# Kernel tuning notes

Measured on AMD Instinct MI355X. Metric: run time of the kernel, lower is better.

## Reference

```python
import jax, jax.numpy as jnp
import numpy as np

B, F, HID, NH, KS, BS = 64, 1024, 2048, 4, 4, 4
HD = HID // NH          # 512 head dim in mLSTMCell
NB = HID // BS          # 512 block-diagonal blocks for q/k/v proj
EPS = 1e-6


def setup_inputs() -> dict:
    key = jax.random.key(0)
    ks = jax.random.split(key, 10)
    r = lambda i, shape, s=0.02: jax.random.normal(ks[i], shape, jnp.float32) * s
    return {
        "inputs": jax.random.normal(ks[0], (B, F), jnp.float32),
        # recurrent carry (zeros_init per _initialize_carry)
        "C": jnp.zeros((B, NH, HD, HD), jnp.float32),
        "n": jnp.zeros((B, NH, HD, 1), jnp.float32),
        "m": jnp.zeros((B, NH, 1, 1), jnp.float32),
        "conv_state": jnp.zeros((B, KS, HID), jnp.float32),
        # parameters
        "W_up": r(1, (F, 2 * HID)),            # up_proj, no bias
        "conv_w": r(2, (KS, HID)),             # depthwise causal conv
        "conv_b": jnp.zeros((HID,), jnp.float32),
        "Wq": r(3, (NB, BS, BS)),              # block-diagonal projections
        "Wk": r(4, (NB, BS, BS)),
        "Wv": r(5, (NB, BS, BS)),
        "Wi": jnp.zeros((3 * HID, NH), jnp.float32),   # gate kernels init to zero
        "bi": jax.random.normal(ks[6], (NH,), jnp.float32) * 0.1,
        "Wf": jnp.zeros((3 * HID, NH), jnp.float32),
        "bf": jnp.linspace(3.0, 6.0, NH, dtype=jnp.float32),  # linspace_init(3,6)
        "norm_scale": jnp.ones((NH, HD), jnp.float32),  # MultiHeadLayerNorm scale
        "skip": jnp.ones((HID,), jnp.float32),          # learnable_skip
        "W_down": r(7, (HID, F)),
    }


def reference(inputs, C, n, m, conv_state, W_up, conv_w, conv_b,
              Wq, Wk, Wv, Wi, bi, Wf, bf, norm_scale, skip, W_down):
    x = inputs[:, None, :]                               # (B,1,F)  add_time_axis
    up = x @ W_up                                        # (B,1,2*HID)
    x, z = jnp.split(up, 2, axis=-1)                     # each (B,1,HID)

    # causal depthwise conv1d, single step: shift state, append x
    conv_state_new = jnp.concatenate([conv_state[:, 1:], x], axis=1)   # (B,KS,HID)
    conv_x = jnp.einsum('bkh,kh->bh', conv_state_new, conv_w)[:, None, :] + conv_b
    conv_x_act = jax.nn.silu(conv_x)                     # (B,1,HID)

    def blockdiag(t, W):  # block-diagonal dense: NB blocks of BSxBS
        tb = t.reshape(B, 1, NB, BS)
        return jnp.einsum('bsnd,nde->bsne', tb, W).reshape(B, 1, HID)

    q = blockdiag(conv_x_act, Wq)
    k = blockdiag(conv_x_act, Wk)
    v = blockdiag(x, Wv)

    # ---- mLSTMCell ----
    qkv = jnp.concatenate([q, k, v], axis=-1)            # (B,1,3*HID)
    qh = q.reshape(B, NH, HD, 1)
    kh = k.reshape(B, NH, HD, 1) / jnp.sqrt(jnp.float32(HD))
    vh = v.reshape(B, NH, HD, 1)

    i_tilde = (qkv @ Wi + bi).swapaxes(-1, -2)[..., None]   # (B,NH,1,1)
    f_tilde = (qkv @ Wf + bf).swapaxes(-1, -2)[..., None]   # (B,NH,1,1)
    log_f = -jax.nn.softplus(-f_tilde)
    m_new = jnp.maximum(log_f + m, i_tilde)
    i_p = jnp.exp(i_tilde - m_new)
    f_p = jnp.exp(log_f + m - m_new)

    C_new = f_p * C + i_p * (kh @ vh.swapaxes(-1, -2))   # rank-1 update (B,NH,HD,HD)
    n_new = f_p * n + i_p * kh                           # (B,NH,HD,1)

    nom = qh.swapaxes(-1, -2) @ C_new                    # (B,NH,1,HD)
    den = jnp.maximum(jnp.abs(qh.swapaxes(-1, -2) @ n_new), jnp.exp(-m_new))
    h_tilde = nom / (den + EPS)                          # (B,NH,1,HD)

    # MultiHeadLayerNorm over head_dim, scale only
    mu = h_tilde.mean(-1, keepdims=True)
    var = h_tilde.var(-1, keepdims=True)
    h_norm = (h_tilde - mu) * jax.lax.rsqrt(var + EPS) * norm_scale[None, :, None, :]
    h_norm = h_norm.swapaxes(1, 2).reshape(B, 1, HID)    # (B,1,HID)
    # ---- end cell ----

    h = h_norm + skip * conv_x_act
    h = h * jax.nn.silu(z)
    y = (h @ W_down)[:, 0]                               # remove_time_axis -> (B,F)
    return (y, C_new, n_new, m_new, conv_state_new)
```

## Files before the change

### kernel.cpp

```cpp
#include <hip/hip_runtime.h>
#include <math.h>

#define BB   64
#define FF   1024
#define HIDD 2048
#define NHH  4
#define KSS  4
#define HDD  512
#define EPSV 1e-6f
#define INV_SQRT_HD 0.04419417382415922f

__global__ __launch_bounds__(256) void k_up_part(const float* __restrict__ A,
                                                 const float* __restrict__ W,
                                                 float* __restrict__ part) {
    const int tid = threadIdx.x;
    const int c  = blockIdx.x * 256 + tid;
    const int b0 = blockIdx.y * 16;
    const int k0 = blockIdx.z * 256;
    __shared__ float As[16 * 256];
#pragma unroll
    for (int j = 0; j < 16; ++j)
        As[j * 256 + tid] = A[(size_t)(b0 + j) * FF + k0 + tid];
    __syncthreads();
    float acc[16];
#pragma unroll
    for (int i = 0; i < 16; ++i) acc[i] = 0.f;
    const float* __restrict__ wp = W + (size_t)k0 * (2 * HIDD) + c;
#pragma unroll 4
    for (int f = 0; f < 256; ++f) {
        const float w = wp[(size_t)f * (2 * HIDD)];
#pragma unroll
        for (int i = 0; i < 16; ++i) acc[i] += As[i * 256 + f] * w;
    }
    float* __restrict__ pp = part + ((size_t)blockIdx.z * BB + b0) * (2 * HIDD) + c;
#pragma unroll
    for (int i = 0; i < 16; ++i) pp[(size_t)i * (2 * HIDD)] = acc[i];
}

__global__ __launch_bounds__(256) void k_up_red(const float* __restrict__ part,
                                                float* __restrict__ up) {
    const int i = (blockIdx.x * 256 + threadIdx.x) * 4;
    float4 s = *(const float4*)(part + i);
#pragma unroll
    for (int kc = 1; kc < 4; ++kc) {
        const float4 p = *(const float4*)(part + (size_t)kc * BB * 2 * HIDD + i);
        s.x += p.x; s.y += p.y; s.z += p.z; s.w += p.w;
    }
    *(float4*)(up + i) = s;
}

__global__ __launch_bounds__(512) void k_conv_qkv(
    const float* __restrict__ up, const float* __restrict__ conv_state,
    const float* __restrict__ conv_w, const float* __restrict__ conv_b,
    const float* __restrict__ Wq, const float* __restrict__ Wk, const float* __restrict__ Wv,
    float* __restrict__ out_cs, float* __restrict__ act,
    float* __restrict__ qb, float* __restrict__ kb, float* __restrict__ vb) {
    const int b  = blockIdx.x;
    const int n  = threadIdx.x;
    const int h0 = n * 4;
    const float4 x4  = *(const float4*)(up + (size_t)b*(2*HIDD) + h0);
    const float4 cs1 = *(const float4*)(conv_state + (size_t)b*KSS*HIDD + 1*HIDD + h0);
    const float4 cs2 = *(const float4*)(conv_state + (size_t)b*KSS*HIDD + 2*HIDD + h0);
    const float4 cs3 = *(const float4*)(conv_state + (size_t)b*KSS*HIDD + 3*HIDD + h0);
    *(float4*)(out_cs + (size_t)b*KSS*HIDD + 0*HIDD + h0) = cs1;
    *(float4*)(out_cs + (size_t)b*KSS*HIDD + 1*HIDD + h0) = cs2;
    *(float4*)(out_cs + (size_t)b*KSS*HIDD + 2*HIDD + h0) = cs3;
    *(float4*)(out_cs + (size_t)b*KSS*HIDD + 3*HIDD + h0) = x4;
    const float4 w0 = *(const float4*)(conv_w + 0*HIDD + h0);
    const float4 w1 = *(const float4*)(conv_w + 1*HIDD + h0);
    const float4 w2 = *(const float4*)(conv_w + 2*HIDD + h0);
    const float4 w3 = *(const float4*)(conv_w + 3*HIDD + h0);
    const float4 cb = *(const float4*)(conv_b + h0);
    float4 cx;
    cx.x = cs1.x*w0.x + cs2.x*w1.x + cs3.x*w2.x + x4.x*w3.x + cb.x;
    cx.y = cs1.y*w0.y + cs2.y*w1.y + cs3.y*w2.y + x4.y*w3.y + cb.y;
    cx.z = cs1.z*w0.z + cs2.z*w1.z + cs3.z*w2.z + x4.z*w3.z + cb.z;
    cx.w = cs1.w*w0.w + cs2.w*w1.w + cs3.w*w2.w + x4.w*w3.w + cb.w;
    float4 a4;
    a4.x = cx.x / (1.f + expf(-cx.x));
    a4.y = cx.y / (1.f + expf(-cx.y));
    a4.z = cx.z / (1.f + expf(-cx.z));
    a4.w = cx.w / (1.f + expf(-cx.w));
    *(float4*)(act + (size_t)b*HIDD + h0) = a4;

    const float4 q0 = *(const float4*)(Wq + (size_t)n*16 + 0);
    const float4 q1 = *(const float4*)(Wq + (size_t)n*16 + 4);
    const float4 q2 = *(const float4*)(Wq + (size_t)n*16 + 8);
    const float4 q3 = *(const float4*)(Wq + (size_t)n*16 + 12);
    float4 q4;
    q4.x = a4.x*q0.x + a4.y*q1.x + a4.z*q2.x + a4.w*q3.x;
    q4.y = a4.x*q0.y + a4.y*q1.y + a4.z*q2.y + a4.w*q3.y;
    q4.z = a4.x*q0.z + a4.y*q1.z + a4.z*q2.z + a4.w*q3.z;
    q4.w = a4.x*q0.w + a4.y*q1.w + a4.z*q2.w + a4.w*q3.w;
    *(float4*)(qb + (size_t)b*HIDD + h0) = q4;
    const float4 k0 = *(const float4*)(Wk + (size_t)n*16 + 0);
    const float4 k1 = *(const float4*)(Wk + (size_t)n*16 + 4);
    const float4 k2 = *(const float4*)(Wk + (size_t)n*16 + 8);
    const float4 k3 = *(const float4*)(Wk + (size_t)n*16 + 12);
    float4 k4;
    k4.x = a4.x*k0.x + a4.y*k1.x + a4.z*k2.x + a4.w*k3.x;
    k4.y = a4.x*k0.y + a4.y*k1.y + a4.z*k2.y + a4.w*k3.y;
    k4.z = a4.x*k0.z + a4.y*k1.z + a4.z*k2.z + a4.w*k3.z;
    k4.w = a4.x*k0.w + a4.y*k1.w + a4.z*k2.w + a4.w*k3.w;
    *(float4*)(kb + (size_t)b*HIDD + h0) = k4;
    const float4 v0 = *(const float4*)(Wv + (size_t)n*16 + 0);
    const float4 v1 = *(const float4*)(Wv + (size_t)n*16 + 4);
    const float4 v2 = *(const float4*)(Wv + (size_t)n*16 + 8);
    const float4 v3 = *(const float4*)(Wv + (size_t)n*16 + 12);
    float4 v4;
    v4.x = x4.x*v0.x + x4.y*v1.x + x4.z*v2.x + x4.w*v3.x;
    v4.y = x4.x*v0.y + x4.y*v1.y + x4.z*v2.y + x4.w*v3.y;
    v4.z = x4.x*v0.z + x4.y*v1.z + x4.z*v2.z + x4.w*v3.z;
    v4.w = x4.x*v0.w + x4.y*v1.w + x4.z*v2.w + x4.w*v3.w;
    *(float4*)(vb + (size_t)b*HIDD + h0) = v4;
}

__global__ __launch_bounds__(256) void k_gates(
    const float* __restrict__ qb, const float* __restrict__ kb, const float* __restrict__ vb,
    const float* __restrict__ Wi, const float* __restrict__ bi,
    const float* __restrict__ Wf, const float* __restrict__ bf,
    const float* __restrict__ mstate_in, const float* __restrict__ nstate_in,
    float* __restrict__ out_m, float* __restrict__ out_n, float* __restrict__ scal) {
    const int bh = blockIdx.x, b = bh >> 2, h = bh & 3;
    const int tid = threadIdx.x;
    __shared__ float r1[256], r2[256];
    __shared__ float bc[3];
    float si = 0.f, sf = 0.f;
    for (int j = tid; j < 3*HIDD; j += 256) {
        const float val = (j < HIDD) ? qb[(size_t)b*HIDD + j]
                        : (j < 2*HIDD) ? kb[(size_t)b*HIDD + j - HIDD]
                                       : vb[(size_t)b*HIDD + j - 2*HIDD];
        si += val * Wi[(size_t)j*NHH + h];
        sf += val * Wf[(size_t)j*NHH + h];
    }
    r1[tid] = si; r2[tid] = sf; __syncthreads();
    for (int s = 128; s > 0; s >>= 1) {
        if (tid < s) { r1[tid] += r1[tid+s]; r2[tid] += r2[tid+s]; }
        __syncthreads();
    }
    if (tid == 0) {
        const float i_t = r1[0] + bi[h];
        const float f_t = r2[0] + bf[h];
        const float log_f = fminf(f_t, 0.f) - log1pf(expf(-fabsf(f_t)));
        const float m_old = mstate_in[bh];
        const float m_new = fmaxf(log_f + m_old, i_t);
        out_m[bh] = m_new;
        bc[0] = expf(log_f + m_old - m_new);
        bc[1] = expf(i_t - m_new) * INV_SQRT_HD;
        bc[2] = expf(-m_new);
    }
    __syncthreads();
    const float f_p = bc[0], ik = bc[1];
    float qn = 0.f;
#pragma unroll
    for (int t = 0; t < 2; ++t) {
        const int d = tid + t*256;
        const float nn = f_p * nstate_in[(size_t)bh*HDD + d] + ik * kb[(size_t)b*HIDD + h*HDD + d];
        out_n[(size_t)bh*HDD + d] = nn;
        qn += qb[(size_t)b*HIDD + h*HDD + d] * nn;
    }
    __syncthreads();
    r1[tid] = qn; __syncthreads();
    for (int s = 128; s > 0; s >>= 1) {
        if (tid < s) r1[tid] += r1[tid+s];
        __syncthreads();
    }
    if (tid == 0) {
        const float den = fmaxf(fabsf(r1[0]), bc[2]);
        scal[bh*4 + 0] = f_p;
        scal[bh*4 + 1] = ik;
        scal[bh*4 + 2] = 1.f / (den + EPSV);
    }
}

__global__ __launch_bounds__(256) void k_cupd(
    const float* __restrict__ C_in, const float* __restrict__ qb,
    const float* __restrict__ kb, const float* __restrict__ vb,
    const float* __restrict__ scal, float* __restrict__ C_out,
    float* __restrict__ nom_part) {
    const int bh = blockIdx.x, rc = blockIdx.y;
    const int b = bh >> 2, h = bh & 3;
    const int tid = threadIdx.x;
    const int c4 = tid & 127, rh = tid >> 7;
    __shared__ float qs[128], ks[128];
    if (tid < 128) qs[tid]      = qb[(size_t)b*HIDD + h*HDD + rc*128 + tid];
    else           ks[tid-128]  = kb[(size_t)b*HIDD + h*HDD + rc*128 + (tid-128)];
    __syncthreads();
    const float f_p = scal[bh*4 + 0], ik = scal[bh*4 + 1];
    const float4 v4 = *(const float4*)(vb + (size_t)b*HIDD + h*HDD + c4*4);
    float4 nom = {0.f,0.f,0.f,0.f};
    const size_t base = ((size_t)bh*HDD + rc*128 + rh*64) * HDD + c4*4;
    const float* __restrict__ cin = C_in + base;
    float* __restrict__ cout = C_out + base;
#pragma unroll 4
    for (int i = 0; i < 64; ++i) {
        const int l = rh*64 + i;
        const float4 c = *(const float4*)(cin + (size_t)i*HDD);
        const float ikk = ik * ks[l];
        float4 cn;
        cn.x = f_p*c.x + ikk*v4.x;
        cn.y = f_p*c.y + ikk*v4.y;
        cn.z = f_p*c.z + ikk*v4.z;
        cn.w = f_p*c.w + ikk*v4.w;
        *(float4*)(cout + (size_t)i*HDD) = cn;
        const float qd = qs[l];
        nom.x += qd*cn.x; nom.y += qd*cn.y; nom.z += qd*cn.z; nom.w += qd*cn.w;
    }
    __shared__ float4 rn[256];
    rn[tid] = nom;
    __syncthreads();
    if (rh == 0) {
        float4 o = rn[tid + 128];
        o.x += nom.x; o.y += nom.y; o.z += nom.z; o.w += nom.w;
        *(float4*)(nom_part + ((size_t)bh*4 + rc)*HDD + c4*4) = o;
    }
}

__global__ __launch_bounds__(256) void k_norm(
    const float* __restrict__ nom_part, const float* __restrict__ scal,
    const float* __restrict__ norm_scale, const float* __restrict__ skip,
    const float* __restrict__ act, const float* __restrict__ up,
    float* __restrict__ hbuf) {
    const int bh = blockIdx.x, b = bh >> 2, h = bh & 3;
    const int tid = threadIdx.x;
    const float invden = scal[bh*4 + 2];
    float ht[2];
    float s = 0.f, sq = 0.f;
#pragma unroll
    for (int t = 0; t < 2; ++t) {
        const int j = tid + t*256;
        float nm = 0.f;
#pragma unroll
        for (int rc = 0; rc < 4; ++rc) nm += nom_part[((size_t)bh*4 + rc)*HDD + j];
        const float v = nm * invden;
        ht[t] = v; s += v; sq += v*v;
    }
    __shared__ float r1[256], r2[256];
    r1[tid] = s; r2[tid] = sq; __syncthreads();
    for (int st = 128; st > 0; st >>= 1) {
        if (tid < st) { r1[tid] += r1[tid+st]; r2[tid] += r2[tid+st]; }
        __syncthreads();
    }
    const float mu = r1[0] * (1.f/HDD);
    const float var = r2[0] * (1.f/HDD) - mu*mu;
    const float rs = rsqrtf(var + EPSV);
#pragma unroll
    for (int t = 0; t < 2; ++t) {
        const int j = tid + t*256;
        const int hid = h*HDD + j;
        const float hn = (ht[t] - mu) * rs * norm_scale[(size_t)h*HDD + j];
        float val = hn + skip[hid] * act[(size_t)b*HIDD + hid];
        const float z = up[(size_t)b*(2*HIDD) + HIDD + hid];
        val *= z / (1.f + expf(-z));
        hbuf[(size_t)b*HIDD + hid] = val;
    }
}

__global__ __launch_bounds__(256) void k_down_part(const float* __restrict__ A,
                                                   const float* __restrict__ W,
                                                   float* __restrict__ part) {
    const int tid = threadIdx.x;
    const int c  = blockIdx.x * 256 + tid;
    const int b0 = blockIdx.y * 16;
    const int k0 = blockIdx.z * 128;
    __shared__ float As[16 * 128];
#pragma unroll
    for (int j = 0; j < 8; ++j) {
        const int e = j * 256 + tid;
        const int i = e >> 7, f = e & 127;
        As[e] = A[(size_t)(b0 + i) * HIDD + k0 + f];
    }
    __syncthreads();
    float acc[16];
#pragma unroll
    for (int i = 0; i < 16; ++i) acc[i] = 0.f;
    const float* __restrict__ wp = W + (size_t)k0 * FF + c;
#pragma unroll 4
    for (int f = 0; f < 128; ++f) {
        const float w = wp[(size_t)f * FF];
#pragma unroll
        for (int i = 0; i < 16; ++i) acc[i] += As[i * 128 + f] * w;
    }
    float* __restrict__ pp = part + ((size_t)blockIdx.z * BB + b0) * FF + c;
#pragma unroll
    for (int i = 0; i < 16; ++i) pp[(size_t)i * FF] = acc[i];
}

__global__ __launch_bounds__(256) void k_down_red(const float* __restrict__ part,
                                                  float* __restrict__ y) {
    const int i = (blockIdx.x * 256 + threadIdx.x) * 4;
    float4 s = *(const float4*)(part + i);
#pragma unroll
    for (int kc = 1; kc < 16; ++kc) {
        const float4 p = *(const float4*)(part + (size_t)kc * BB * FF + i);
        s.x += p.x; s.y += p.y; s.z += p.z; s.w += p.w;
    }
    *(float4*)(y + i) = s;
}

extern "C" void kernel_launch(void* const* d_in, const int* in_sizes, int n_in,
                              void* d_out, int out_size, void* d_ws, size_t ws_size,
                              hipStream_t stream) {
    const float* inputs     = (const float*)d_in[0];
    const float* C_in       = (const float*)d_in[1];
    const float* nstate_in  = (const float*)d_in[2];
    const float* mstate_in  = (const float*)d_in[3];
    const float* conv_state = (const float*)d_in[4];
    const float* W_up       = (const float*)d_in[5];
    const float* conv_w     = (const float*)d_in[6];
    const float* conv_b     = (const float*)d_in[7];
    const float* Wq         = (const float*)d_in[8];
    const float* Wk         = (const float*)d_in[9];
    const float* Wv         = (const float*)d_in[10];
    const float* Wi         = (const float*)d_in[11];
    const float* bi         = (const float*)d_in[12];
    const float* Wf         = (const float*)d_in[13];
    const float* bf         = (const float*)d_in[14];
    const float* norm_scale = (const float*)d_in[15];
    const float* skip       = (const float*)d_in[16];
    const float* W_down     = (const float*)d_in[17];

    float* ws = (float*)d_ws;
    float* up       = ws;
    float* act      = ws + 262144;
    float* qb       = ws + 393216;
    float* kb       = ws + 524288;
    float* vb       = ws + 655360;
    float* scal     = ws + 786432;
    float* nom_part = ws + 787456;
    float* hbuf     = ws + 1311744;
    float* part_up  = ws + 1442816;
    float* part_y   = ws + 2491392;

    float* out_y  = (float*)d_out;
    float* out_C  = out_y + 65536;
    float* out_n  = out_C + 67108864;
    float* out_m  = out_n + 131072;
    float* out_cs = out_m + 256;

    k_up_part <<<dim3(16, 4, 4), 256, 0, stream>>>(inputs, W_up, part_up);
    k_up_red  <<<256,            256, 0, stream>>>(part_up, up);
    k_conv_qkv<<<BB,             512, 0, stream>>>(up, conv_state, conv_w, conv_b,
                                                   Wq, Wk, Wv, out_cs, act, qb, kb, vb);
    k_gates   <<<BB*NHH,         256, 0, stream>>>(qb, kb, vb, Wi, bi, Wf, bf,
                                                   mstate_in, nstate_in, out_m, out_n, scal);
    k_cupd    <<<dim3(BB*NHH, 4), 256, 0, stream>>>(C_in, qb, kb, vb, scal, out_C, nom_part);
    k_norm    <<<BB*NHH,         256, 0, stream>>>(nom_part, scal, norm_scale, skip, act, up, hbuf);
    k_down_part<<<dim3(4, 4, 16), 256, 0, stream>>>(hbuf, W_down, part_y);
    k_down_red <<<64,            256, 0, stream>>>(part_y, out_y);
}
```

Before: 576.1 us.

## Fuse mid-pipeline kernels: up-reduce into conv/qkv/gates, C-update into norm

Folds the up-projection split-K reduction, conv, q/k/v projection, gate computation and n-state update into one per-batch kernel that uses wave shuffles for its reductions. The C rank-1 update is merged with the layer norm and output gating in a 512-thread block per (batch, head), which removes the nom_part round trip. The two GEMM inner loops are also vectorised to read float4 from shared memory. Going from eight launches to five cuts launch overhead and intermediate traffic, but the C update now runs on 256 blocks instead of 1024, which may reduce memory-level parallelism on the dominant 256MB stream.

```diff
diff --git a/kernel.cpp b/kernel.cpp
--- a/kernel.cpp
+++ b/kernel.cpp
@@ -26,233 +26,262 @@
 #pragma unroll
     for (int i = 0; i < 16; ++i) acc[i] = 0.f;
     const float* __restrict__ wp = W + (size_t)k0 * (2 * HIDD) + c;
-#pragma unroll 4
-    for (int f = 0; f < 256; ++f) {
-        const float w = wp[(size_t)f * (2 * HIDD)];
-#pragma unroll
-        for (int i = 0; i < 16; ++i) acc[i] += As[i * 256 + f] * w;
+#pragma unroll 2
+    for (int f4 = 0; f4 < 64; ++f4) {
+        const float w0 = wp[(size_t)(4*f4 + 0) * (2 * HIDD)];
+        const float w1 = wp[(size_t)(4*f4 + 1) * (2 * HIDD)];
+        const float w2 = wp[(size_t)(4*f4 + 2) * (2 * HIDD)];
+        const float w3 = wp[(size_t)(4*f4 + 3) * (2 * HIDD)];
+#pragma unroll
+        for (int i = 0; i < 16; ++i) {
+            const float4 a = *(const float4*)(As + i * 256 + f4 * 4);
+            acc[i] += a.x * w0 + a.y * w1 + a.z * w2 + a.w * w3;
+        }
     }
     float* __restrict__ pp = part + ((size_t)blockIdx.z * BB + b0) * (2 * HIDD) + c;
 #pragma unroll
     for (int i = 0; i < 16; ++i) pp[(size_t)i * (2 * HIDD)] = acc[i];
 }
 
-__global__ __launch_bounds__(256) void k_up_red(const float* __restrict__ part,
-                                                float* __restrict__ up) {
-    const int i = (blockIdx.x * 256 + threadIdx.x) * 4;
-    float4 s = *(const float4*)(part + i);
-#pragma unroll
-    for (int kc = 1; kc < 4; ++kc) {
-        const float4 p = *(const float4*)(part + (size_t)kc * BB * 2 * HIDD + i);
-        s.x += p.x; s.y += p.y; s.z += p.z; s.w += p.w;
-    }
-    *(float4*)(up + i) = s;
-}
-
-__global__ __launch_bounds__(512) void k_conv_qkv(
-    const float* __restrict__ up, const float* __restrict__ conv_state,
+__global__ __launch_bounds__(512) void k_mid(
+    const float* __restrict__ part_up, const float* __restrict__ conv_state,
     const float* __restrict__ conv_w, const float* __restrict__ conv_b,
     const float* __restrict__ Wq, const float* __restrict__ Wk, const float* __restrict__ Wv,
-    float* __restrict__ out_cs, float* __restrict__ act,
-    float* __restrict__ qb, float* __restrict__ kb, float* __restrict__ vb) {
+    const float* __restrict__ Wi, const float* __restrict__ bi,
+    const float* __restrict__ Wf, const float* __restrict__ bf,
+    const float* __restrict__ mstate_in, const float* __restrict__ nstate_in,
+    const float* __restrict__ skip,
+    float* __restrict__ out_cs, float* __restrict__ out_m, float* __restrict__ out_n,
+    float* __restrict__ sact, float* __restrict__ zsil,
+    float* __restrict__ qb, float* __restrict__ kb, float* __restrict__ vb,
+    float* __restrict__ scal) {
     const int b  = blockIdx.x;
     const int n  = threadIdx.x;
     const int h0 = n * 4;
-    const float4 x4  = *(const float4*)(up + (size_t)b*(2*HIDD) + h0);
-    const float4 cs1 = *(const float4*)(conv_state + (size_t)b*KSS*HIDD + 1*HIDD + h0);
-    const float4 cs2 = *(const float4*)(conv_state + (size_t)b*KSS*HIDD + 2*HIDD + h0);
-    const float4 cs3 = *(const float4*)(conv_state + (size_t)b*KSS*HIDD + 3*HIDD + h0);
-    *(float4*)(out_cs + (size_t)b*KSS*HIDD + 0*HIDD + h0) = cs1;
-    *(float4*)(out_cs + (size_t)b*KSS*HIDD + 1*HIDD + h0) = cs2;
-    *(float4*)(out_cs + (size_t)b*KSS*HIDD + 2*HIDD + h0) = cs3;
-    *(float4*)(out_cs + (size_t)b*KSS*HIDD + 3*HIDD + h0) = x4;
-    const float4 w0 = *(const float4*)(conv_w + 0*HIDD + h0);
-    const float4 w1 = *(const float4*)(conv_w + 1*HIDD + h0);
-    const float4 w2 = *(const float4*)(conv_w + 2*HIDD + h0);
-    const float4 w3 = *(const float4*)(conv_w + 3*HIDD + h0);
-    const float4 cb = *(const float4*)(conv_b + h0);
+
+    float4 x4 = *(const float4*)(part_up + (size_t)b * (2 * HIDD) + h0);
+#pragma unroll
+    for (int kc = 1; kc < 4; ++kc) {
+        const float4 p = *(const float4*)(part_up + ((size_t)kc * BB + b) * (2 * HIDD) + h0);
+        x4.x += p.x; x4.y += p.y; x4.z += p.z; x4.w += p.w;
+    }
+    float4 z4 = *(const float4*)(part_up + (size_t)b * (2 * HIDD) + HIDD + h0);
+#pragma unroll
+    for (int kc = 1; kc < 4; ++kc) {
+        const float4 p = *(const float4*)(part_up + ((size_t)kc * BB + b) * (2 * HIDD) + HIDD + h0);
+        z4.x += p.x; z4.y += p.y; z4.z += p.z; z4.w += p.w;
+    }
+    float4 zs;
+    zs.x = z4.x / (1.f + expf(-z4.x));
+    zs.y = z4.y / (1.f + expf(-z4.y));
+    zs.z = z4.z / (1.f + expf(-z4.z));
+    zs.w = z4.w / (1.f + expf(-z4.w));
+    *(float4*)(zsil + (size_t)b * HIDD + h0) = zs;
+
+    const float4 cs1 = *(const float4*)(conv_state + (size_t)b * KSS * HIDD + 1 * HIDD + h0);
+    const float4 cs2 = *(const float4*)(conv_state + (size_t)b * KSS * HIDD + 2 * HIDD + h0);
+    const float4 cs3 = *(const float4*)(conv_state + (size_t)b * KSS * HIDD + 3 * HIDD + h0);
+    *(float4*)(out_cs + (size_t)b * KSS * HIDD + 0 * HIDD + h0) = cs1;
+    *(float4*)(out_cs + (size_t)b * KSS * HIDD + 1 * HIDD + h0) = cs2;
+    *(float4*)(out_cs + (size_t)b * KSS * HIDD + 2 * HIDD + h0) = cs3;
+    *(float4*)(out_cs + (size_t)b * KSS * HIDD + 3 * HIDD + h0) = x4;
+    const float4 cw0 = *(const float4*)(conv_w + 0 * HIDD + h0);
+    const float4 cw1 = *(const float4*)(conv_w + 1 * HIDD + h0);
+    const float4 cw2 = *(const float4*)(conv_w + 2 * HIDD + h0);
+    const float4 cw3 = *(const float4*)(conv_w + 3 * HIDD + h0);
+    const float4 cb  = *(const float4*)(conv_b + h0);
     float4 cx;
-    cx.x = cs1.x*w0.x + cs2.x*w1.x + cs3.x*w2.x + x4.x*w3.x + cb.x;
-    cx.y = cs1.y*w0.y + cs2.y*w1.y + cs3.y*w2.y + x4.y*w3.y + cb.y;
-    cx.z = cs1.z*w0.z + cs2.z*w1.z + cs3.z*w2.z + x4.z*w3.z + cb.z;
-    cx.w = cs1.w*w0.w + cs2.w*w1.w + cs3.w*w2.w + x4.w*w3.w + cb.w;
+    cx.x = cs1.x*cw0.x + cs2.x*cw1.x + cs3.x*cw2.x + x4.x*cw3.x + cb.x;
+    cx.y = cs1.y*cw0.y + cs2.y*cw1.y + cs3.y*cw2.y + x4.y*cw3.y + cb.y;
+    cx.z = cs1.z*cw0.z + cs2.z*cw1.z + cs3.z*cw2.z + x4.z*cw3.z + cb.z;
+    cx.w = cs1.w*cw0.w + cs2.w*cw1.w + cs3.w*cw2.w + x4.w*cw3.w + cb.w;
     float4 a4;
     a4.x = cx.x / (1.f + expf(-cx.x));
     a4.y = cx.y / (1.f + expf(-cx.y));
     a4.z = cx.z / (1.f + expf(-cx.z));
     a4.w = cx.w / (1.f + expf(-cx.w));
-    *(float4*)(act + (size_t)b*HIDD + h0) = a4;
-
-    const float4 q0 = *(const float4*)(Wq + (size_t)n*16 + 0);
-    const float4 q1 = *(const float4*)(Wq + (size_t)n*16 + 4);
-    const float4 q2 = *(const float4*)(Wq + (size_t)n*16 + 8);
-    const float4 q3 = *(const float4*)(Wq + (size_t)n*16 + 12);
-    float4 q4;
-    q4.x = a4.x*q0.x + a4.y*q1.x + a4.z*q2.x + a4.w*q3.x;
-    q4.y = a4.x*q0.y + a4.y*q1.y + a4.z*q2.y + a4.w*q3.y;
-    q4.z = a4.x*q0.z + a4.y*q1.z + a4.z*q2.z + a4.w*q3.z;
-    q4.w = a4.x*q0.w + a4.y*q1.w + a4.z*q2.w + a4.w*q3.w;
-    *(float4*)(qb + (size_t)b*HIDD + h0) = q4;
-    const float4 k0 = *(const float4*)(Wk + (size_t)n*16 + 0);
-    const float4 k1 = *(const float4*)(Wk + (size_t)n*16 + 4);
-    const float4 k2 = *(const float4*)(Wk + (size_t)n*16 + 8);
-    const float4 k3 = *(const float4*)(Wk + (size_t)n*16 + 12);
-    float4 k4;
-    k4.x = a4.x*k0.x + a4.y*k1.x + a4.z*k2.x + a4.w*k3.x;
-    k4.y = a4.x*k0.y + a4.y*k1.y + a4.z*k2.y + a4.w*k3.y;
-    k4.z = a4.x*k0.z + a4.y*k1.z + a4.z*k2.z + a4.w*k3.z;
-    k4.w = a4.x*k0.w + a4.y*k1.w + a4.z*k2.w + a4.w*k3.w;
-    *(float4*)(kb + (size_t)b*HIDD + h0) = k4;
-    const float4 v0 = *(const float4*)(Wv + (size_t)n*16 + 0);
-    const float4 v1 = *(const float4*)(Wv + (size_t)n*16 + 4);
-    const float4 v2 = *(const float4*)(Wv + (size_t)n*16 + 8);
-    const float4 v3 = *(const float4*)(Wv + (size_t)n*16 + 12);
-    float4 v4;
-    v4.x = x4.x*v0.x + x4.y*v1.x + x4.z*v2.x + x4.w*v3.x;
-    v4.y = x4.x*v0.y + x4.y*v1.y + x4.z*v2.y + x4.w*v3.y;
-    v4.z = x4.x*v0.z + x4.y*v1.z + x4.z*v2.z + x4.w*v3.z;
-    v4.w = x4.x*v0.w + x4.y*v1.w + x4.z*v2.w + x4.w*v3.w;
-    *(float4*)(vb + (size_t)b*HIDD + h0) = v4;
-}
-
-__global__ __launch_bounds__(256) void k_gates(
-    const float* __restrict__ qb, const float* __restrict__ kb, const float* __restrict__ vb,
-    const float* __restrict__ Wi, const float* __restrict__ bi,
-    const float* __restrict__ Wf, const float* __restrict__ bf,
-    const float* __restrict__ mstate_in, const float* __restrict__ nstate_in,
-    float* __restrict__ out_m, float* __restrict__ out_n, float* __restrict__ scal) {
+    const float4 sk = *(const float4*)(skip + h0);
+    float4 sa;
+    sa.x = sk.x * a4.x; sa.y = sk.y * a4.y; sa.z = sk.z * a4.z; sa.w = sk.w * a4.w;
+    *(float4*)(sact + (size_t)b * HIDD + h0) = sa;
+
+    const float4 q0 = *(const float4*)(Wq + (size_t)n * 16 + 0);
+    const float4 q1 = *(const float4*)(Wq + (size_t)n * 16 + 4);
+    const float4 q2 = *(const float4*)(Wq + (size_t)n * 16 + 8);
+    const float4 q3 = *(const float4*)(Wq + (size_t)n * 16 + 12);
+    float4 qv4;
+    qv4.x = a4.x*q0.x + a4.y*q1.x + a4.z*q2.x + a4.w*q3.x;
+    qv4.y = a4.x*q0.y + a4.y*q1.y + a4.z*q2.y + a4.w*q3.y;
+    qv4.z = a4.x*q0.z + a4.y*q1.z + a4.z*q2.z + a4.w*q3.z;
+    qv4.w = a4.x*q0.w + a4.y*q1.w + a4.z*q2.w + a4.w*q3.w;
+    *(float4*)(qb + (size_t)b * HIDD + h0) = qv4;
+    const float4 k0v = *(const float4*)(Wk + (size_t)n * 16 + 0);
+    const float4 k1v = *(const float4*)(Wk + (size_t)n * 16 + 4);
+    const float4 k2v = *(const float4*)(Wk + (size_t)n * 16 + 8);
+    const float4 k3v = *(const float4*)(Wk + (size_t)n * 16 + 12);
+    float4 kv4;
+    kv4.x = a4.x*k0v.x + a4.y*k1v.x + a4.z*k2v.x + a4.w*k3v.x;
+    kv4.y = a4.x*k0v.y + a4.y*k1v.y + a4.z*k2v.y + a4.w*k3v.y;
+    kv4.z = a4.x*k0v.z + a4.y*k1v.z + a4.z*k2v.z + a4.w*k3v.z;
+    kv4.w = a4.x*k0v.w + a4.y*k1v.w + a4.z*k2v.w + a4.w*k3v.w;
+    *(float4*)(kb + (size_t)b * HIDD + h0) = kv4;
+    const float4 v0 = *(const float4*)(Wv + (size_t)n * 16 + 0);
+    const float4 v1 = *(const float4*)(Wv + (size_t)n * 16 + 4);
+    const float4 v2 = *(const float4*)(Wv + (size_t)n * 16 + 8);
+    const float4 v3 = *(const float4*)(Wv + (size_t)n * 16 + 12);
+    float4 vv4;
+    vv4.x = x4.x*v0.x + x4.y*v1.x + x4.z*v2.x + x4.w*v3.x;
+    vv4.y = x4.x*v0.y + x4.y*v1.y + x4.z*v2.y + x4.w*v3.y;
+    vv4.z = x4.x*v0.z + x4.y*v1.z + x4.z*v2.z + x4.w*v3.z;
+    vv4.w = x4.x*v0.w + x4.y*v1.w + x4.z*v2.w + x4.w*v3.w;
+    *(float4*)(vb + (size_t)b * HIDD + h0) = vv4;
+
+    float si0 = 0.f, si1 = 0.f, si2 = 0.f, si3 = 0.f;
+    float sf0 = 0.f, sf1 = 0.f, sf2 = 0.f, sf3 = 0.f;
+#define GATE_R(comp, r) { \
+    const float qr = qv4.comp, kr = kv4.comp, vr = vv4.comp; \
+    const float4 wq_ = *(const float4*)(Wi + (size_t)(h0 + (r)) * NHH); \
+    const float4 wk_ = *(const float4*)(Wi + (size_t)(HIDD + h0 + (r)) * NHH); \
+    const float4 wv_ = *(const float4*)(Wi + (size_t)(2*HIDD + h0 + (r)) * NHH); \
+    si0 += qr*wq_.x + kr*wk_.x + vr*wv_.x; \
+    si1 += qr*wq_.y + kr*wk_.y + vr*wv_.y; \
+    si2 += qr*wq_.z + kr*wk_.z + vr*wv_.z; \
+    si3 += qr*wq_.w + kr*wk_.w + vr*wv_.w; \
+    const float4 fq_ = *(const float4*)(Wf + (size_t)(h0 + (r)) * NHH); \
+    const float4 fk_ = *(const float4*)(Wf + (size_t)(HIDD + h0 + (r)) * NHH); \
+    const float4 fv_ = *(const float4*)(Wf + (size_t)(2*HIDD + h0 + (r)) * NHH); \
+    sf0 += qr*fq_.x + kr*fk_.x + vr*fv_.x; \
+    sf1 += qr*fq_.y + kr*fk_.y + vr*fv_.y; \
+    sf2 += qr*fq_.z + kr*fk_.z + vr*fv_.z; \
+    sf3 += qr*fq_.w + kr*fk_.w + vr*fv_.w; \
+}
+    GATE_R(x, 0) GATE_R(y, 1) GATE_R(z, 2) GATE_R(w, 3)
+#undef GATE_R
+#pragma unroll
+    for (int off = 32; off > 0; off >>= 1) {
+        si0 += __shfl_down(si0, off); si1 += __shfl_down(si1, off);
+        si2 += __shfl_down(si2, off); si3 += __shfl_down(si3, off);
+        sf0 += __shfl_down(sf0, off); sf1 += __shfl_down(sf1, off);
+        sf2 += __shfl_down(sf2, off); sf3 += __shfl_down(sf3, off);
+    }
+    const int lane = n & 63, wv = n >> 6;
+    __shared__ float Ls[8][8];
+    if (lane == 0) {
+        Ls[wv][0] = si0; Ls[wv][1] = si1; Ls[wv][2] = si2; Ls[wv][3] = si3;
+        Ls[wv][4] = sf0; Ls[wv][5] = sf1; Ls[wv][6] = sf2; Ls[wv][7] = sf3;
+    }
+    __syncthreads();
+    __shared__ float bcst[4][3];
+    if (n < 4) {
+        float it = bi[n], ft = bf[n];
+#pragma unroll
+        for (int w = 0; w < 8; ++w) { it += Ls[w][n]; ft += Ls[w][4 + n]; }
+        const float log_f = fminf(ft, 0.f) - log1pf(expf(-fabsf(ft)));
+        const float m_old = mstate_in[b * NHH + n];
+        const float m_new = fmaxf(log_f + m_old, it);
+        out_m[b * NHH + n] = m_new;
+        const float f_p = expf(log_f + m_old - m_new);
+        const float ikv = expf(it - m_new) * INV_SQRT_HD;
+        bcst[n][0] = f_p; bcst[n][1] = ikv; bcst[n][2] = expf(-m_new);
+        float* sc = scal + (size_t)(b * NHH + n) * 4;
+        sc[0] = f_p; sc[1] = ikv;
+    }
+    __syncthreads();
+
+    const int h  = n >> 7;
+    const int bh = b * NHH + h;
+    const float f_p = bcst[h][0], ikv = bcst[h][1];
+    const int d0 = (n & 127) * 4;
+    const float4 nin = *(const float4*)(nstate_in + (size_t)bh * HDD + d0);
+    float4 nn;
+    nn.x = f_p * nin.x + ikv * kv4.x;
+    nn.y = f_p * nin.y + ikv * kv4.y;
+    nn.z = f_p * nin.z + ikv * kv4.z;
+    nn.w = f_p * nin.w + ikv * kv4.w;
+    *(float4*)(out_n + (size_t)bh * HDD + d0) = nn;
+    float qn = qv4.x * nn.x + qv4.y * nn.y + qv4.z * nn.z + qv4.w * nn.w;
+#pragma unroll
+    for (int off = 32; off > 0; off >>= 1) qn += __shfl_down(qn, off);
+    __shared__ float qnl[8];
+    if (lane == 0) qnl[wv] = qn;
+    __syncthreads();
+    if (n < 4) {
+        const float den = fmaxf(fabsf(qnl[2 * n] + qnl[2 * n + 1]), bcst[n][2]);
+        scal[(size_t)(b * NHH + n) * 4 + 2] = 1.f / (den + EPSV);
+    }
+}
+
+__global__ __launch_bounds__(512) void k_cupd_norm(
+    const float* __restrict__ C_in, const float* __restrict__ qb,
+    const float* __restrict__ kb, const float* __restrict__ vb,
+    const float* __restrict__ scal, const float* __restrict__ norm_scale,
+    const float* __restrict__ sact, const float* __restrict__ zsil,
+    float* __restrict__ C_out, float* __restrict__ hbuf) {
     const int bh = blockIdx.x, b = bh >> 2, h = bh & 3;
     const int tid = threadIdx.x;
-    __shared__ float r1[256], r2[256];
-    __shared__ float bc[3];
-    float si = 0.f, sf = 0.f;
-    for (int j = tid; j < 3*HIDD; j += 256) {
-        const float val = (j < HIDD) ? qb[(size_t)b*HIDD + j]
-                        : (j < 2*HIDD) ? kb[(size_t)b*HIDD + j - HIDD]
-                                       : vb[(size_t)b*HIDD + j - 2*HIDD];
-        si += val * Wi[(size_t)j*NHH + h];
-        sf += val * Wf[(size_t)j*NHH + h];
-    }
-    r1[tid] = si; r2[tid] = sf; __syncthreads();
-    for (int s = 128; s > 0; s >>= 1) {
-        if (tid < s) { r1[tid] += r1[tid+s]; r2[tid] += r2[tid+s]; }
-        __syncthreads();
-    }
-    if (tid == 0) {
-        const float i_t = r1[0] + bi[h];
-        const float f_t = r2[0] + bf[h];
-        const float log_f = fminf(f_t, 0.f) - log1pf(expf(-fabsf(f_t)));
-        const float m_old = mstate_in[bh];
-        const float m_new = fmaxf(log_f + m_old, i_t);
-        out_m[bh] = m_new;
-        bc[0] = expf(log_f + m_old - m_new);
-        bc[1] = expf(i_t - m_new) * INV_SQRT_HD;
-        bc[2] = expf(-m_new);
-    }
-    __syncthreads();
-    const float f_p = bc[0], ik = bc[1];
-    float qn = 0.f;
-#pragma unroll
-    for (int t = 0; t < 2; ++t) {
-        const int d = tid + t*256;
-        const float nn = f_p * nstate_in[(size_t)bh*HDD + d] + ik * kb[(size_t)b*HIDD + h*HDD + d];
-        out_n[(size_t)bh*HDD + d] = nn;
-        qn += qb[(size_t)b*HIDD + h*HDD + d] * nn;
-    }
-    __syncthreads();
-    r1[tid] = qn; __syncthreads();
-    for (int s = 128; s > 0; s >>= 1) {
-        if (tid < s) r1[tid] += r1[tid+s];
-        __syncthreads();
-    }
-    if (tid == 0) {
-        const float den = fmaxf(fabsf(r1[0]), bc[2]);
-        scal[bh*4 + 0] = f_p;
-        scal[bh*4 + 1] = ik;
-        scal[bh*4 + 2] = 1.f / (den + EPSV);
-    }
-}
-
-__global__ __launch_bounds__(256) void k_cupd(
-    const float* __restrict__ C_in, const float* __restrict__ qb,
-    const float* __restrict__ kb, const float* __restrict__ vb,
-    const float* __restrict__ scal, float* __restrict__ C_out,
-    float* __restrict__ nom_part) {
-    const int bh = blockIdx.x, rc = blockIdx.y;
-    const int b = bh >> 2, h = bh & 3;
-    const int tid = threadIdx.x;
-    const int c4 = tid & 127, rh = tid >> 7;
-    __shared__ float qs[128], ks[128];
-    if (tid < 128) qs[tid]      = qb[(size_t)b*HIDD + h*HDD + rc*128 + tid];
-    else           ks[tid-128]  = kb[(size_t)b*HIDD + h*HDD + rc*128 + (tid-128)];
-    __syncthreads();
-    const float f_p = scal[bh*4 + 0], ik = scal[bh*4 + 1];
-    const float4 v4 = *(const float4*)(vb + (size_t)b*HIDD + h*HDD + c4*4);
-    float4 nom = {0.f,0.f,0.f,0.f};
-    const size_t base = ((size_t)bh*HDD + rc*128 + rh*64) * HDD + c4*4;
-    const float* __restrict__ cin = C_in + base;
+    const int c4 = tid & 127, rg = tid >> 7;
+    __shared__ float qs[HDD], kik[HDD];
+    const float f_p    = scal[bh * 4 + 0];
+    const float ikv    = scal[bh * 4 + 1];
+    const float invden = scal[bh * 4 + 2];
+    qs[tid]  = qb[(size_t)b * HIDD + h * HDD + tid];
+    kik[tid] = ikv * kb[(size_t)b * HIDD + h * HDD + tid];
+    __syncthreads();
+    const float4 v4 = *(const float4*)(vb + (size_t)b * HIDD + h * HDD + c4 * 4);
+    float4 nom = {0.f, 0.f, 0.f, 0.f};
+    const size_t base = ((size_t)bh * HDD + rg * 128) * HDD + c4 * 4;
+    const float* __restrict__ cin  = C_in  + base;
     float* __restrict__ cout = C_out + base;
-#pragma unroll 4
-    for (int i = 0; i < 64; ++i) {
-        const int l = rh*64 + i;
-        const float4 c = *(const float4*)(cin + (size_t)i*HDD);
-        const float ikk = ik * ks[l];
+#pragma unroll 8
+    for (int i = 0; i < 128; ++i) {
+        const float4 c = *(const float4*)(cin + (size_t)i * HDD);
+        const float kk = kik[rg * 128 + i];
         float4 cn;
-        cn.x = f_p*c.x + ikk*v4.x;
-        cn.y = f_p*c.y + ikk*v4.y;
-        cn.z = f_p*c.z + ikk*v4.z;
-        cn.w = f_p*c.w + ikk*v4.w;
-        *(float4*)(cout + (size_t)i*HDD) = cn;
-        const float qd = qs[l];
-        nom.x += qd*cn.x; nom.y += qd*cn.y; nom.z += qd*cn.z; nom.w += qd*cn.w;
-    }
-    __shared__ float4 rn[256];
+        cn.x = f_p * c.x + kk * v4.x;
+        cn.y = f_p * c.y + kk * v4.y;
+        cn.z = f_p * c.z + kk * v4.z;
+        cn.w = f_p * c.w + kk * v4.w;
+        *(float4*)(cout + (size_t)i * HDD) = cn;
+        const float qd = qs[rg * 128 + i];
+        nom.x += qd * cn.x; nom.y += qd * cn.y; nom.z += qd * cn.z; nom.w += qd * cn.w;
+    }
+    __shared__ float4 rn[512];
     rn[tid] = nom;
     __syncthreads();
-    if (rh == 0) {
-        float4 o = rn[tid + 128];
-        o.x += nom.x; o.y += nom.y; o.z += nom.z; o.w += nom.w;
-        *(float4*)(nom_part + ((size_t)bh*4 + rc)*HDD + c4*4) = o;
-    }
-}
-
-__global__ __launch_bounds__(256) void k_norm(
-    const float* __restrict__ nom_part, const float* __restrict__ scal,
-    const float* __restrict__ norm_scale, const float* __restrict__ skip,
-    const float* __restrict__ act, const float* __restrict__ up,
-    float* __restrict__ hbuf) {
-    const int bh = blockIdx.x, b = bh >> 2, h = bh & 3;
-    const int tid = threadIdx.x;
-    const float invden = scal[bh*4 + 2];
-    float ht[2];
-    float s = 0.f, sq = 0.f;
-#pragma unroll
-    for (int t = 0; t < 2; ++t) {
-        const int j = tid + t*256;
-        float nm = 0.f;
-#pragma unroll
-        for (int rc = 0; rc < 4; ++rc) nm += nom_part[((size_t)bh*4 + rc)*HDD + j];
-        const float v = nm * invden;
-        ht[t] = v; s += v; sq += v*v;
-    }
-    __shared__ float r1[256], r2[256];
-    r1[tid] = s; r2[tid] = sq; __syncthreads();
-    for (int st = 128; st > 0; st >>= 1) {
-        if (tid < st) { r1[tid] += r1[tid+st]; r2[tid] += r2[tid+st]; }
-        __syncthreads();
-    }
-    const float mu = r1[0] * (1.f/HDD);
-    const float var = r2[0] * (1.f/HDD) - mu*mu;
-    const float rs = rsqrtf(var + EPSV);
-#pragma unroll
-    for (int t = 0; t < 2; ++t) {
-        const int j = tid + t*256;
-        const int hid = h*HDD + j;
-        const float hn = (ht[t] - mu) * rs * norm_scale[(size_t)h*HDD + j];
-        float val = hn + skip[hid] * act[(size_t)b*HIDD + hid];
-        const float z = up[(size_t)b*(2*HIDD) + HIDD + hid];
-        val *= z / (1.f + expf(-z));
-        hbuf[(size_t)b*HIDD + hid] = val;
+    __shared__ float Ls[2], Ls2[2];
+    float4 ht = {0.f, 0.f, 0.f, 0.f};
+    if (rg == 0) {
+#pragma unroll
+        for (int g = 1; g < 4; ++g) {
+            const float4 o = rn[g * 128 + tid];
+            nom.x += o.x; nom.y += o.y; nom.z += o.z; nom.w += o.w;
+        }
+        ht.x = nom.x * invden; ht.y = nom.y * invden;
+        ht.z = nom.z * invden; ht.w = nom.w * invden;
+        float s  = ht.x + ht.y + ht.z + ht.w;
+        float sq = ht.x*ht.x + ht.y*ht.y + ht.z*ht.z + ht.w*ht.w;
+#pragma unroll
+        for (int off = 32; off > 0; off >>= 1) {
+            s  += __shfl_down(s, off);
+            sq += __shfl_down(sq, off);
+        }
+        if ((tid & 63) == 0) { Ls[tid >> 6] = s; Ls2[tid >> 6] = sq; }
+    }
+    __syncthreads();
+    if (rg == 0) {
+        const float mu  = (Ls[0] + Ls[1]) * (1.f / HDD);
+        const float var = (Ls2[0] + Ls2[1]) * (1.f / HDD) - mu * mu;
+        const float rs  = rsqrtf(var + EPSV);
+        const size_t o = (size_t)b * HIDD + h * HDD + c4 * 4;
+        const float4 nsc = *(const float4*)(norm_scale + (size_t)h * HDD + c4 * 4);
+        const float4 sa  = *(const float4*)(sact + o);
+        const float4 zs  = *(const float4*)(zsil + o);
+        float4 val;
+        val.x = ((ht.x - mu) * rs * nsc.x + sa.x) * zs.x;
+        val.y = ((ht.y - mu) * rs * nsc.y + sa.y) * zs.y;
+        val.z = ((ht.z - mu) * rs * nsc.z + sa.z) * zs.z;
+        val.w = ((ht.w - mu) * rs * nsc.w + sa.w) * zs.w;
+        *(float4*)(hbuf + o) = val;
     }
 }
 
@@ -275,11 +304,17 @@
 #pragma unroll
     for (int i = 0; i < 16; ++i) acc[i] = 0.f;
     const float* __restrict__ wp = W + (size_t)k0 * FF + c;
-#pragma unroll 4
-    for (int f = 0; f < 128; ++f) {
-        const float w = wp[(size_t)f * FF];
-#pragma unroll
-        for (int i = 0; i < 16; ++i) acc[i] += As[i * 128 + f] * w;
+#pragma unroll 2
+    for (int f4 = 0; f4 < 32; ++f4) {
+        const float w0 = wp[(size_t)(4*f4 + 0) * FF];
+        const float w1 = wp[(size_t)(4*f4 + 1) * FF];
+        const float w2 = wp[(size_t)(4*f4 + 2) * FF];
+        const float w3 = wp[(size_t)(4*f4 + 3) * FF];
+#pragma unroll
+        for (int i = 0; i < 16; ++i) {
+            const float4 a = *(const float4*)(As + i * 128 + f4 * 4);
+            acc[i] += a.x * w0 + a.y * w1 + a.z * w2 + a.w * w3;
+        }
     }
     float* __restrict__ pp = part + ((size_t)blockIdx.z * BB + b0) * FF + c;
 #pragma unroll
@@ -321,16 +356,15 @@
     const float* W_down     = (const float*)d_in[17];
 
     float* ws = (float*)d_ws;
-    float* up       = ws;
-    float* act      = ws + 262144;
-    float* qb       = ws + 393216;
-    float* kb       = ws + 524288;
-    float* vb       = ws + 655360;
-    float* scal     = ws + 786432;
-    float* nom_part = ws + 787456;
-    float* hbuf     = ws + 1311744;
-    float* part_up  = ws + 1442816;
-    float* part_y   = ws + 2491392;
+    float* part_up = ws;
+    float* sact    = ws + 1048576;
+    float* zsil    = sact + 131072;
+    float* qb      = zsil + 131072;
+    float* kb      = qb   + 131072;
+    float* vb      = kb   + 131072;
+    float* scal    = vb   + 131072;
+    float* hbuf    = scal + 1024;
+    float* part_y  = hbuf + 131072;
 
     float* out_y  = (float*)d_out;
     float* out_C  = out_y + 65536;
@@ -338,14 +372,14 @@
     float* out_m  = out_n + 131072;
     float* out_cs = out_m + 256;
 
-    k_up_part <<<dim3(16, 4, 4), 256, 0, stream>>>(inputs, W_up, part_up);
-    k_up_red  <<<256,            256, 0, stream>>>(part_up, up);
-    k_conv_qkv<<<BB,             512, 0, stream>>>(up, conv_state, conv_w, conv_b,
-                                                   Wq, Wk, Wv, out_cs, act, qb, kb, vb);
-    k_gates   <<<BB*NHH,         256, 0, stream>>>(qb, kb, vb, Wi, bi, Wf, bf,
-                                                   mstate_in, nstate_in, out_m, out_n, scal);
-    k_cupd    <<<dim3(BB*NHH, 4), 256, 0, stream>>>(C_in, qb, kb, vb, scal, out_C, nom_part);
-    k_norm    <<<BB*NHH,         256, 0, stream>>>(nom_part, scal, norm_scale, skip, act, up, hbuf);
+    k_up_part  <<<dim3(16, 4, 4), 256, 0, stream>>>(inputs, W_up, part_up);
+    k_mid      <<<BB,             512, 0, stream>>>(part_up, conv_state, conv_w, conv_b,
+                                                    Wq, Wk, Wv, Wi, bi, Wf, bf,
+                                                    mstate_in, nstate_in, skip,
+                                                    out_cs, out_m, out_n,
+                                                    sact, zsil, qb, kb, vb, scal);
+    k_cupd_norm<<<BB * NHH,       512, 0, stream>>>(C_in, qb, kb, vb, scal, norm_scale,
+                                                    sact, zsil, out_C, hbuf);
     k_down_part<<<dim3(4, 4, 16), 256, 0, stream>>>(hbuf, W_down, part_y);
-    k_down_red <<<64,            256, 0, stream>>>(part_y, out_y);
-}
+    k_down_red <<<64,             256, 0, stream>>>(part_y, out_y);
+}
```

Result: no change. 580.0 us (+0.7%).
